# Kernel optimization log

Hardware: AMD Instinct MI355X
Metric: run time of the kernel (lower is better)

## Reference

```python
import jax, jax.numpy as jnp
import numpy as np

H = 1024        # bridge_hidden_dim
NH = 16         # num_attention_heads
HD = H // NH    # head_dim = 64
B, S = 4, 1024
PHYS_W = 0.2
CONS_W = 0.15


def setup_inputs() -> dict:
    key = jax.random.key(0)
    ks = jax.random.split(key, 16)
    sc = 0.02
    return {
        "cnn_features": jax.random.normal(ks[0], (B, S, H), jnp.float32),
        "llm_features": jax.random.normal(ks[1], (B, S, H), jnp.float32),
        "Wq": jax.random.normal(ks[2], (H, H), jnp.float32) * sc,
        "bq": jnp.zeros((H,), jnp.float32),
        "Wk": jax.random.normal(ks[3], (H, H), jnp.float32) * sc,
        "bk": jnp.zeros((H,), jnp.float32),
        "Wv": jax.random.normal(ks[4], (H, H), jnp.float32) * sc,
        "bv": jnp.zeros((H,), jnp.float32),
        "Wo": jax.random.normal(ks[5], (H, H), jnp.float32) * sc,
        "bo": jnp.zeros((H,), jnp.float32),
        "ln_g": jnp.ones((H,), jnp.float32),
        "ln_b": jnp.zeros((H,), jnp.float32),
        "e_energy": jax.random.normal(ks[6], (H,), jnp.float32),
        "e_mass": jax.random.normal(ks[7], (H,), jnp.float32),
        "e_momentum": jax.random.normal(ks[8], (H,), jnp.float32),
    }


def _layernorm(x, g, b, eps=1e-5):
    mu = jnp.mean(x, axis=-1, keepdims=True)
    var = jnp.var(x, axis=-1, keepdims=True)
    return (x - mu) * jax.lax.rsqrt(var + eps) * g + b


def _split_heads(x):
    b, s, _ = x.shape
    return x.reshape(b, s, NH, HD).transpose(0, 2, 1, 3)  # [b, h, s, d]


def _physics_attention(q_in, k_in, v_in, Wq, bq, Wk, bk, Wv, bv, Wo, bo, ln_g, ln_b):
    # q_in: [b, sq, H]; k_in == v_in: [b, sk, H] with sq == sk (required by bias math)
    Q = _split_heads(q_in @ Wq.T + bq)  # [b,h,s,d]
    K = _split_heads(k_in @ Wk.T + bk)
    V = _split_heads(v_in @ Wv.T + bv)
    scores = jnp.einsum('bhqd,bhkd->bhqk', Q, K) / jnp.sqrt(jnp.float32(HD))
    # physics constraints (broadcast [b,h,s,1] over key axis)
    energy_bias = jnp.sum(Q * K, axis=-1, keepdims=True) * PHYS_W
    mass_bias = jnp.mean(Q + K, axis=-1, keepdims=True) * CONS_W
    scores = scores + energy_bias + mass_bias
    attn = jax.nn.softmax(scores, axis=-1)  # dropout is identity in eval
    att = jnp.einsum('bhqk,bhkd->bhqd', attn, V)
    b, h, s, d = att.shape
    att = att.transpose(0, 2, 1, 3).reshape(b, s, h * d)
    out = att @ Wo.T + bo
    return _layernorm(q_in + out, ln_g, ln_b)


def reference(cnn_features, llm_features, Wq, bq, Wk, bk, Wv, bv, Wo, bo,
              ln_g, ln_b, e_energy, e_mass, e_momentum):
    b = cnn_features.shape[0]
    phys = jnp.stack([e_energy, e_mass, e_momentum], axis=0)  # [3, H]
    phys = jnp.broadcast_to(phys[None], (b, 3, H))
    aug_cnn = jnp.concatenate([cnn_features, phys], axis=1)  # [b, S+3, H]
    aug_llm = jnp.concatenate([llm_features, phys], axis=1)
    cnn_att = _physics_attention(aug_cnn, aug_llm, aug_llm,
                                 Wq, bq, Wk, bk, Wv, bv, Wo, bo, ln_g, ln_b)
    llm_att = _physics_attention(aug_llm, aug_cnn, aug_cnn,
                                 Wq, bq, Wk, bk, Wv, bv, Wo, bo, ln_g, ln_b)
    cnn_out = cnn_att[:, :cnn_features.shape[1], :]
    llm_out = llm_att[:, :llm_features.shape[1], :]
    return (cnn_out, llm_out)
```

## Files before the change

kernel.cpp:

```cpp
#include <hip/hip_runtime.h>
#include <stdint.h>

#define SA 1027
#define MROWS 8216
#define MPAD 8448
#define SPAD 1088
#define ATTM 8192

typedef __attribute__((ext_vector_type(8))) short short8;
typedef __attribute__((ext_vector_type(4))) float f32x4;
typedef __attribute__((ext_vector_type(2))) unsigned int u32x2;

typedef const __attribute__((address_space(1))) uint8_t* gas1;
typedef __attribute__((address_space(3))) uint8_t* las3;

__device__ __forceinline__ void gload16(const void* g, void* l){
  __builtin_amdgcn_global_load_lds((gas1)g, (las3)l, 16, 0, 0);
}

__device__ __forceinline__ uint16_t f2bf(float f){
  uint32_t x = __builtin_bit_cast(uint32_t, f);
  x = (x + 0x7fffu + ((x >> 16) & 1u)) >> 16;
  return (uint16_t)x;
}
__device__ __forceinline__ float bf2f(uint16_t u){
  uint32_t x = ((uint32_t)u) << 16;
  return __builtin_bit_cast(float, x);
}

__device__ __forceinline__ f32x4 mfma16(short8 a, short8 b, f32x4 c){
  return __builtin_amdgcn_mfma_f32_16x16x32_bf16(a, b, c, 0, 0, 0);
}

#define QSCALE 0.18033688011112042f

__global__ __launch_bounds__(256) void prep_wb(
    const float* __restrict__ Wq, const float* __restrict__ Wk,
    const float* __restrict__ Wv, const float* __restrict__ Wo,
    const float* __restrict__ bq, const float* __restrict__ bk,
    const float* __restrict__ bv, const float* __restrict__ bo,
    uint16_t* __restrict__ W, float* __restrict__ bias){
  const int gid = blockIdx.x*256 + threadIdx.x;
  if (gid < 1048576){
    const int w = gid >> 18;
    const int off = (gid & 262143) << 2;
    const float* src = (w==0) ? Wq : (w==1) ? Wk : (w==2) ? Wv : Wo;
    const float4 v = *(const float4*)(src + off);
    ushort4 u;
    u.x = f2bf(v.x); u.y = f2bf(v.y); u.z = f2bf(v.z); u.w = f2bf(v.w);
    *(ushort4*)(W + ((size_t)w << 20) + off) = u;
  } else if (gid < 1048576 + 1024){
    const int i = (gid - 1048576) << 2;
    const int w = i >> 10;
    const int off = i & 1023;
    const float* src = (w==0) ? bq : (w==1) ? bk : (w==2) ? bv : bo;
    *(float4*)(bias + i) = *(const float4*)(src + off);
  }
}

__global__ __launch_bounds__(256) void prep_X(
    const float* __restrict__ cnn, const float* __restrict__ llm,
    const float* __restrict__ ee, const float* __restrict__ em,
    const float* __restrict__ ep, uint16_t* __restrict__ X){
  const int row = blockIdx.x;
  const int c4 = threadIdx.x << 2;
  float4 v = {0.f,0.f,0.f,0.f};
  if (row < MROWS){
    const int cb = row / SA;
    const int s = row - cb*SA;
    const int c = cb >> 2, b = cb & 3;
    const float* src;
    if (s < 1024) src = (c ? llm : cnn) + ((size_t)(b*1024 + s))*1024 + c4;
    else src = ((s == 1024) ? ee : (s == 1025) ? em : ep) + c4;
    v = *(const float4*)src;
  }
  ushort4 u;
  u.x = f2bf(v.x); u.y = f2bf(v.y); u.z = f2bf(v.z); u.w = f2bf(v.w);
  *(ushort4*)(X + (size_t)row*1024 + c4) = u;
}

__global__ __launch_bounds__(512) void gemm256k(
    const uint16_t* __restrict__ A, const uint16_t* __restrict__ B,
    const float* __restrict__ bias, uint16_t* __restrict__ C,
    int K, int lda, int ldb, int ldc, int nbn, float qscale, int qcols){
  extern __shared__ uint8_t lds[];
  const int tid = threadIdx.x;
  const int lane = tid & 63, wid = tid >> 6;
  const int l15 = lane & 15, l4 = lane >> 4;
  const int wm = wid >> 2, wn = wid & 3;
  const int nwg = gridDim.x;
  const int q8 = nwg >> 3, r8 = nwg & 7;
  const int xcd = blockIdx.x & 7, loc = blockIdx.x >> 3;
  const int wg = (xcd < r8 ? xcd*(q8+1) : r8*(q8+1) + (xcd-r8)*q8) + loc;
  const int bm = wg / nbn, bn = wg % nbn;

  const uint16_t* Ag = A + (size_t)bm*256*lda;
  const uint16_t* Bg = B + (size_t)bn*256*ldb;

  const int srow8 = lane >> 3;
  const int gch = (lane & 7) ^ srow8;
  const int c0 = wid*2, c1 = c0 + 1;
  const size_t ga0 = (size_t)(c0*8 + srow8)*lda + gch*8;
  const size_t ga1 = (size_t)(c1*8 + srow8)*lda + gch*8;
  const size_t gb0 = (size_t)(c0*8 + srow8)*ldb + gch*8;
  const size_t gb1 = (size_t)(c1*8 + srow8)*ldb + gch*8;

#define STG_A(buf, H, kt) do { \
    gload16(Ag + (size_t)(H)*128*lda + (size_t)(kt)*64 + ga0, lds + (buf)*65536 + (H)*16384 + c0*1024); \
    gload16(Ag + (size_t)(H)*128*lda + (size_t)(kt)*64 + ga1, lds + (buf)*65536 + (H)*16384 + c1*1024); \
  } while(0)
#define STG_B(buf, H, kt) do { \
    gload16(Bg + (size_t)(H)*128*ldb + (size_t)(kt)*64 + gb0, lds + (buf)*65536 + 32768 + (H)*16384 + c0*1024); \
    gload16(Bg + (size_t)(H)*128*ldb + (size_t)(kt)*64 + gb1, lds + (buf)*65536 + 32768 + (H)*16384 + c1*1024); \
  } while(0)

  int koff[2];
  koff[0] = (l4*16) ^ ((l15 & 7) << 4);
  koff[1] = (64 + l4*16) ^ ((l15 & 7) << 4);
  const int arow = (wm*128 + l15) * 128;
  const int brow = (wn*64 + l15) * 128;

  f32x4 acc[8][4];
  #pragma unroll
  for (int i = 0; i < 8; ++i)
    #pragma unroll
    for (int j = 0; j < 4; ++j) acc[i][j] = (f32x4){0.f,0.f,0.f,0.f};

  const int NT = K >> 6;
  STG_A(0,0,0); STG_A(0,1,0); STG_B(0,0,0); STG_B(0,1,0);
  STG_B(1,0,1); STG_B(1,1,1);
  asm volatile("s_waitcnt vmcnt(4)" ::: "memory");
  __builtin_amdgcn_s_barrier();

  for (int s = 0; s < NT; ++s){
    const int b = s & 1;
    const uint8_t* La = lds + b*65536;
    const uint8_t* Lb = La + 32768;
    const int sn1 = (s+1 < NT) ? s+1 : s;
    const int sn2 = (s+2 < NT) ? s+2 : s;
    const int nb = b ^ 1;
    short8 af[4][2], bf0[2][2], bf1[2][2];

    #pragma unroll
    for (int i = 0; i < 4; ++i){
      af[i][0] = *(const short8*)(La + arow + i*2048 + koff[0]);
      af[i][1] = *(const short8*)(La + arow + i*2048 + koff[1]);
    }
    #pragma unroll
    for (int j = 0; j < 2; ++j){
      bf0[j][0] = *(const short8*)(Lb + brow + j*2048 + koff[0]);
      bf0[j][1] = *(const short8*)(Lb + brow + j*2048 + koff[1]);
    }
    STG_A(nb, 0, sn1);
    __builtin_amdgcn_s_barrier();
    asm volatile("s_waitcnt lgkmcnt(0)" ::: "memory");
    __builtin_amdgcn_sched_barrier(0);
    __builtin_amdgcn_s_setprio(1);
    #pragma unroll
    for (int i = 0; i < 4; ++i)
      #pragma unroll
      for (int j = 0; j < 2; ++j)
        acc[i][j] = mfma16(af[i][1], bf0[j][1], mfma16(af[i][0], bf0[j][0], acc[i][j]));
    __builtin_amdgcn_s_setprio(0);
    __builtin_amdgcn_s_barrier();

    #pragma unroll
    for (int j = 0; j < 2; ++j){
      bf1[j][0] = *(const short8*)(Lb + brow + (j+2)*2048 + koff[0]);
      bf1[j][1] = *(const short8*)(Lb + brow + (j+2)*2048 + koff[1]);
    }
    STG_A(nb, 1, sn1);
    __builtin_amdgcn_s_barrier();
    asm volatile("s_waitcnt lgkmcnt(0)" ::: "memory");
    __builtin_amdgcn_sched_barrier(0);
    __builtin_amdgcn_s_setprio(1);
    #pragma unroll
    for (int i = 0; i < 4; ++i)
      #pragma unroll
      for (int j = 0; j < 2; ++j)
        acc[i][j+2] = mfma16(af[i][1], bf1[j][1], mfma16(af[i][0], bf1[j][0], acc[i][j+2]));
    __builtin_amdgcn_s_setprio(0);
    __builtin_amdgcn_s_barrier();

    #pragma unroll
    for (int i = 0; i < 4; ++i){
      af[i][0] = *(const short8*)(La + 8192 + arow + i*2048 + koff[0]);
      af[i][1] = *(const short8*)(La + 8192 + arow + i*2048 + koff[1]);
    }
    STG_B(b, 0, sn2);
    __builtin_amdgcn_s_barrier();
    asm volatile("s_waitcnt lgkmcnt(0)" ::: "memory");
    __builtin_amdgcn_sched_barrier(0);
    __builtin_amdgcn_s_setprio(1);
    #pragma unroll
    for (int i = 0; i < 4; ++i)
      #pragma unroll
      for (int j = 0; j < 2; ++j)
        acc[i+4][j+2] = mfma16(af[i][1], bf1[j][1], mfma16(af[i][0], bf1[j][0], acc[i+4][j+2]));
    __builtin_amdgcn_s_setprio(0);
    __builtin_amdgcn_s_barrier();

    STG_B(b, 1, sn2);
    __builtin_amdgcn_s_barrier();
    __builtin_amdgcn_s_setprio(1);
    #pragma unroll
    for (int i = 0; i < 4; ++i)
      #pragma unroll
      for (int j = 0; j < 2; ++j)
        acc[i+4][j] = mfma16(af[i][1], bf0[j][1], mfma16(af[i][0], bf0[j][0], acc[i+4][j]));
    __builtin_amdgcn_s_setprio(0);
    asm volatile("s_waitcnt vmcnt(4)" ::: "memory");
    __builtin_amdgcn_s_barrier();
  }

  #pragma unroll
  for (int j = 0; j < 4; ++j){
    const int n = bn*256 + wn*64 + j*16 + l15;
    const float bb = bias[n];
    const float sc = (n < qcols) ? qscale : 1.0f;
    #pragma unroll
    for (int i = 0; i < 8; ++i){
      const size_t m0 = (size_t)bm*256 + wm*128 + i*16 + l4*4;
      #pragma unroll
      for (int r = 0; r < 4; ++r)
        C[(m0 + r)*ldc + n] = f2bf((acc[i][j][r] + bb) * sc);
    }
  }
#undef STG_A
#undef STG_B
}

__global__ __launch_bounds__(256) void vtrans(
    const uint16_t* __restrict__ Y, uint16_t* __restrict__ Vt){
  __shared__ uint16_t t[64][65];
  const int bid = blockIdx.x;
  const int st = bid % 17, cbh = bid / 17;
  const int s0 = st*64;
  const int tid = threadIdx.x;
  const int a = tid >> 2, g = tid & 3;
  const int cb = cbh >> 4, h = cbh & 15;
  const int s = s0 + a;
  short8 v0 = {0,0,0,0,0,0,0,0}, v1 = {0,0,0,0,0,0,0,0};
  if (s < SA){
    const uint16_t* p = Y + ((size_t)cb*SA + s)*3072 + 2048 + h*64 + g*16;
    v0 = *(const short8*)p;
    v1 = *(const short8*)(p + 8);
  }
  #pragma unroll
  for (int i=0;i<8;i++){ t[a][g*16+i] = (uint16_t)v0[i]; t[a][g*16+8+i] = (uint16_t)v1[i]; }
  __syncthreads();
  short8 w0, w1;
  #pragma unroll
  for (int i=0;i<8;i++){ w0[i] = (short)t[g*16+i][a]; w1[i] = (short)t[g*16+8+i][a]; }
  uint16_t* o = Vt + ((size_t)cbh*64 + a)*SPAD + s0 + g*16;
  *(short8*)o = w0;
  *(short8*)(o + 8) = w1;
}

__global__ __launch_bounds__(256, 4) void attn_k(
    const uint16_t* __restrict__ Y, const uint16_t* __restrict__ Vt,
    uint16_t* __restrict__ att){
  __shared__ __align__(16) uint8_t smK[16384];
  __shared__ __align__(16) uint8_t smV[16384];
  __shared__ __align__(16) uint8_t smP[8192];
  const int tid = threadIdx.x;
  const int lane = tid & 63, wid = tid >> 6;
  const int l15 = lane & 15, l4 = lane >> 4;
  const int i = blockIdx.x;
  const int inst = (i & 7) * 16 + (i >> 6);
  const int qb = (i >> 3) & 7;
  const int h = inst & 15, cb = inst >> 4;
  const size_t yrow0 = (size_t)cb * SA;
  const int q0 = qb * 128 + wid * 32;
  const size_t vbase = (size_t)inst * 64 * SPAD;
  const uint16_t* Yk = Y + yrow0 * 3072 + 1024 + h * 64;

  short8 qf[2][2];
  #pragma unroll
  for (int u = 0; u < 2; ++u){
    const uint16_t* p = Y + (yrow0 + q0 + u*16 + l15) * 3072 + h * 64 + l4 * 8;
    qf[u][0] = *(const short8*)p;
    qf[u][1] = *(const short8*)(p + 32);
  }

  f32x4 o0[4], o1[4];
  float psum0 = 0.f, psum1 = 0.f;
  #pragma unroll
  for (int d = 0; d < 4; ++d){ o0[d] = (f32x4){0,0,0,0}; o1[d] = (f32x4){0,0,0,0}; }

  int koff[2], pwo[4];
  #pragma unroll
  for (int kk = 0; kk < 2; ++kk)
    koff[kk] = (l15*128 + kk*64 + l4*16) ^ ((l15 & 7) << 4);
  #pragma unroll
  for (int nt = 0; nt < 4; ++nt)
    pwo[nt] = (l15*128 + nt*32 + l4*8) ^ ((l15 & 7) << 4);
  uint8_t* const pb = smP + wid * 2048;

  const int srow = lane >> 3, schunk = lane & 7;
  #pragma unroll
  for (int j = 0; j < 2; ++j){
    const int cj = wid*2 + j;
    const int row = cj*8 + srow;
    const int gch = schunk ^ (row & 7);
    gload16(Yk + (size_t)row * 3072 + gch*8, smK + cj*1024);
    gload16(Vt + vbase + (size_t)row * SPAD + gch*8, smV + cj*1024);
  }
  __syncthreads();

  int cur = 0;
  for (int kt = 0; kt < 17; ++kt){
    if (kt < 16){
      const int s1n = (kt + 1) * 64;
      const int nb = (cur ^ 1) * 8192;
      #pragma unroll
      for (int j = 0; j < 2; ++j){
        const int cj = wid*2 + j;
        const int row = cj*8 + srow;
        const int gch = schunk ^ (row & 7);
        gload16(Yk + (size_t)(s1n + row) * 3072 + gch*8, smK + nb + cj*1024);
        gload16(Vt + vbase + (size_t)row * SPAD + s1n + gch*8, smV + nb + cj*1024);
      }
    }
    const uint8_t* bK = smK + cur * 8192;
    const uint8_t* bV = smV + cur * 8192;

    f32x4 sa[4], sb[4];
    #pragma unroll
    for (int nt = 0; nt < 4; ++nt){
      const short8 k0 = *(const short8*)(bK + nt*2048 + koff[0]);
      const short8 k1 = *(const short8*)(bK + nt*2048 + koff[1]);
      sa[nt] = mfma16(k1, qf[0][1], mfma16(k0, qf[0][0], (f32x4){0,0,0,0}));
      sb[nt] = mfma16(k1, qf[1][1], mfma16(k0, qf[1][0], (f32x4){0,0,0,0}));
    }
    if (kt == 16){
      #pragma unroll
      for (int nt = 0; nt < 4; ++nt)
        #pragma unroll
        for (int r = 0; r < 4; ++r){
          if (nt*16 + l4*4 + r >= 3){ sa[nt][r] = -3e38f; sb[nt][r] = -3e38f; }
        }
    }
    #pragma unroll
    for (int nt = 0; nt < 4; ++nt){
      const float p0 = __builtin_amdgcn_exp2f(sa[nt][0]);
      const float p1 = __builtin_amdgcn_exp2f(sa[nt][1]);
      const float p2 = __builtin_amdgcn_exp2f(sa[nt][2]);
      const float p3 = __builtin_amdgcn_exp2f(sa[nt][3]);
      psum0 += (p0 + p1) + (p2 + p3);
      uint32_t w0, w1;
      asm("v_cvt_pk_bf16_f32 %0, %1, %2" : "=v"(w0) : "v"(p0), "v"(p1));
      asm("v_cvt_pk_bf16_f32 %0, %1, %2" : "=v"(w1) : "v"(p2), "v"(p3));
      *(u32x2*)(pb + pwo[nt]) = (u32x2){w0, w1};
    }
    short8 vf[4][2];
    #pragma unroll
    for (int dt = 0; dt < 4; ++dt){
      vf[dt][0] = *(const short8*)(bV + dt*2048 + koff[0]);
      vf[dt][1] = *(const short8*)(bV + dt*2048 + koff[1]);
    }
    #pragma unroll
    for (int kk = 0; kk < 2; ++kk){
      const short8 pf = *(const short8*)(pb + koff[kk]);
      #pragma unroll
      for (int dt = 0; dt < 4; ++dt)
        o0[dt] = mfma16(pf, vf[dt][kk], o0[dt]);
    }
    #pragma unroll
    for (int nt = 0; nt < 4; ++nt){
      const float p0 = __builtin_amdgcn_exp2f(sb[nt][0]);
      const float p1 = __builtin_amdgcn_exp2f(sb[nt][1]);
      const float p2 = __builtin_amdgcn_exp2f(sb[nt][2]);
      const float p3 = __builtin_amdgcn_exp2f(sb[nt][3]);
      psum1 += (p0 + p1) + (p2 + p3);
      uint32_t w0, w1;
      asm("v_cvt_pk_bf16_f32 %0, %1, %2" : "=v"(w0) : "v"(p0), "v"(p1));
      asm("v_cvt_pk_bf16_f32 %0, %1, %2" : "=v"(w1) : "v"(p2), "v"(p3));
      *(u32x2*)(pb + pwo[nt]) = (u32x2){w0, w1};
    }
    #pragma unroll
    for (int kk = 0; kk < 2; ++kk){
      const short8 pf = *(const short8*)(pb + koff[kk]);
      #pragma unroll
      for (int dt = 0; dt < 4; ++dt)
        o1[dt] = mfma16(pf, vf[dt][kk], o1[dt]);
    }
    __syncthreads();
    cur ^= 1;
  }

  psum0 += __shfl_xor(psum0, 16); psum0 += __shfl_xor(psum0, 32);
  psum1 += __shfl_xor(psum1, 16); psum1 += __shfl_xor(psum1, 32);
  const size_t arow0 = (size_t)cb * 1024 + q0;
  #pragma unroll
  for (int r = 0; r < 4; ++r){
    const float inv0 = 1.f / __shfl(psum0, l4*4 + r);
    const float inv1 = 1.f / __shfl(psum1, l4*4 + r);
    #pragma unroll
    for (int dt = 0; dt < 4; ++dt){
      att[(arow0 + l4*4 + r)*1024 + h*64 + dt*16 + l15] = f2bf(o0[dt][r] * inv0);
      att[(arow0 + 16 + l4*4 + r)*1024 + h*64 + dt*16 + l15] = f2bf(o1[dt][r] * inv1);
    }
  }
}

__global__ __launch_bounds__(256) void ln_out(
    const uint16_t* __restrict__ Op, const float* __restrict__ cnn,
    const float* __restrict__ llm, const float* __restrict__ g,
    const float* __restrict__ b, float* __restrict__ out){
  const int row = blockIdx.x;
  const int c = row >> 12, bq = row & 4095;
  const int tid = threadIdx.x;
  const ushort4 u = *(const ushort4*)(Op + (size_t)row*1024 + (tid<<2));
  const float4 rv = *(const float4*)((c ? llm : cnn) + (size_t)bq*1024 + (tid<<2));
  const float x0 = bf2f(u.x) + rv.x;
  const float x1 = bf2f(u.y) + rv.y;
  const float x2 = bf2f(u.z) + rv.z;
  const float x3 = bf2f(u.w) + rv.w;
  float s1 = x0+x1+x2+x3;
  float s2 = x0*x0+x1*x1+x2*x2+x3*x3;
  #pragma unroll
  for (int m=1;m<64;m<<=1){ s1 += __shfl_xor(s1,m); s2 += __shfl_xor(s2,m); }
  __shared__ float r1[4], r2[4];
  const int wid = tid >> 6, lane = tid & 63;
  if (lane == 0){ r1[wid] = s1; r2[wid] = s2; }
  __syncthreads();
  s1 = r1[0]+r1[1]+r1[2]+r1[3];
  s2 = r2[0]+r2[1]+r2[2]+r2[3];
  const float mu = s1 * 0.0009765625f;
  const float var = s2 * 0.0009765625f - mu*mu;
  const float rs = rsqrtf(var + 1e-5f);
  const float4 gv = *(const float4*)(g + (tid<<2));
  const float4 bv = *(const float4*)(b + (tid<<2));
  float4 ov;
  ov.x = (x0 - mu)*rs*gv.x + bv.x;
  ov.y = (x1 - mu)*rs*gv.y + bv.y;
  ov.z = (x2 - mu)*rs*gv.z + bv.z;
  ov.w = (x3 - mu)*rs*gv.w + bv.w;
  *(float4*)(out + ((size_t)c << 22) + (size_t)bq*1024 + (tid<<2)) = ov;
}

extern "C" void kernel_launch(void* const* d_in, const int* in_sizes, int n_in,
                              void* d_out, int out_size, void* d_ws, size_t ws_size,
                              hipStream_t stream){
  const float* cnn = (const float*)d_in[0];
  const float* llm = (const float*)d_in[1];
  const float* Wq  = (const float*)d_in[2];
  const float* bq  = (const float*)d_in[3];
  const float* Wk  = (const float*)d_in[4];
  const float* bk  = (const float*)d_in[5];
  const float* Wv  = (const float*)d_in[6];
  const float* bv  = (const float*)d_in[7];
  const float* Wo  = (const float*)d_in[8];
  const float* bo  = (const float*)d_in[9];
  const float* lng = (const float*)d_in[10];
  const float* lnb = (const float*)d_in[11];
  const float* ee  = (const float*)d_in[12];
  const float* em  = (const float*)d_in[13];
  const float* ep  = (const float*)d_in[14];

  uint8_t* ws = (uint8_t*)d_ws;
  uint16_t* X    = (uint16_t*)(ws + 0);
  uint16_t* W    = (uint16_t*)(ws + 17301504);
  float*    bias = (float*)   (ws + 25690112);
  uint16_t* Y    = (uint16_t*)(ws + 25706496);
  uint16_t* Vt   = (uint16_t*)(ws + 77611008);
  uint16_t* att  = X;
  uint16_t* Op   = Y;
  float* out = (float*)d_out;

  hipFuncSetAttribute((const void*)gemm256k,
                      hipFuncAttributeMaxDynamicSharedMemorySize, 131072);

  prep_wb<<<4100, 256, 0, stream>>>(Wq, Wk, Wv, Wo, bq, bk, bv, bo, W, bias);
  prep_X<<<MPAD, 256, 0, stream>>>(cnn, llm, ee, em, ep, X);
  gemm256k<<<396, 512, 131072, stream>>>(X, W, bias, Y, 1024, 1024, 1024, 3072, 12, QSCALE, 1024);
  vtrans<<<128*17, 256, 0, stream>>>(Y, Vt);
  attn_k<<<1024, 256, 0, stream>>>(Y, Vt, att);
  gemm256k<<<128, 512, 131072, stream>>>(att, W + 3145728, bias + 3072, Op, 1024, 1024, 1024, 1024, 4, 1.0f, 0);
  ln_out<<<ATTM, 256, 0, stream>>>(Op, cnn, llm, lng, lnb, out);
}
```

Before: 184.1 us.

## Fuse V transpose into QKV GEMM epilogue and split physics rows into separate kernel

The QKV GEMM moves from 256x256 to 256x128 tiles, which gives more workgroups. Its epilogue now writes Q/K into a 2048-wide buffer and V directly in transposed layout, so the separate vtrans kernel is removed. The three physics token rows are computed by a small dedicated GEMV kernel, which shrinks the main GEMM M dimension to exactly 8192 with no padding. The attention kernel uses 512-thread blocks covering 256 queries each to share K/V staging across more waves. This trades a larger per-block footprint and an extra tiny launch for one fewer full pass over V.

```diff
diff --git a/kernel.cpp b/kernel.cpp
--- a/kernel.cpp
+++ b/kernel.cpp
@@ -2,10 +2,7 @@
 #include <stdint.h>
 
 #define SA 1027
-#define MROWS 8216
-#define MPAD 8448
 #define SPAD 1088
-#define ATTM 8192
 
 typedef __attribute__((ext_vector_type(8))) short short8;
 typedef __attribute__((ext_vector_type(4))) float f32x4;
@@ -60,29 +57,53 @@
 
 __global__ __launch_bounds__(256) void prep_X(
     const float* __restrict__ cnn, const float* __restrict__ llm,
-    const float* __restrict__ ee, const float* __restrict__ em,
-    const float* __restrict__ ep, uint16_t* __restrict__ X){
+    uint16_t* __restrict__ X){
   const int row = blockIdx.x;
   const int c4 = threadIdx.x << 2;
-  float4 v = {0.f,0.f,0.f,0.f};
-  if (row < MROWS){
-    const int cb = row / SA;
-    const int s = row - cb*SA;
-    const int c = cb >> 2, b = cb & 3;
-    const float* src;
-    if (s < 1024) src = (c ? llm : cnn) + ((size_t)(b*1024 + s))*1024 + c4;
-    else src = ((s == 1024) ? ee : (s == 1025) ? em : ep) + c4;
-    v = *(const float4*)src;
-  }
+  const int cb = row >> 10, s = row & 1023;
+  const int c = cb >> 2, b = cb & 3;
+  const float4 v = *(const float4*)((c ? llm : cnn) + ((size_t)(b*1024 + s))*1024 + c4);
   ushort4 u;
   u.x = f2bf(v.x); u.y = f2bf(v.y); u.z = f2bf(v.z); u.w = f2bf(v.w);
   *(ushort4*)(X + (size_t)row*1024 + c4) = u;
 }
 
-__global__ __launch_bounds__(512) void gemm256k(
+__global__ __launch_bounds__(256) void phys_qkv(
+    const float* __restrict__ ee, const float* __restrict__ em,
+    const float* __restrict__ ep, const uint16_t* __restrict__ W,
+    const float* __restrict__ bias, uint16_t* __restrict__ Yqk,
+    uint16_t* __restrict__ Vt){
+  __shared__ float xs[1024];
+  const int t = blockIdx.x >> 3;
+  const int col = 1024 + (blockIdx.x & 7)*256 + threadIdx.x;
+  const float* e = (t==0) ? ee : (t==1) ? em : ep;
+  for (int k = threadIdx.x; k < 1024; k += 256) xs[k] = bf2f(f2bf(e[k]));
+  __syncthreads();
+  const uint16_t* wr = W + (size_t)col*1024;
+  float acc = 0.f;
+  for (int k = 0; k < 1024; k += 8){
+    const short8 w8 = *(const short8*)(wr + k);
+    #pragma unroll
+    for (int u = 0; u < 8; ++u) acc += bf2f((uint16_t)w8[u]) * xs[k+u];
+  }
+  const uint16_t o = f2bf(acc + bias[col]);
+  if (col < 2048){
+    #pragma unroll
+    for (int cb = 0; cb < 8; ++cb)
+      Yqk[((size_t)cb*SA + 1024 + t)*2048 + col] = o;
+  } else {
+    const int hd = col - 2048;
+    #pragma unroll
+    for (int cb = 0; cb < 8; ++cb)
+      Vt[((size_t)(cb*1024 + hd))*SPAD + 1024 + t] = o;
+  }
+}
+
+__global__ __launch_bounds__(512) void gemm256x128(
     const uint16_t* __restrict__ A, const uint16_t* __restrict__ B,
     const float* __restrict__ bias, uint16_t* __restrict__ C,
-    int K, int lda, int ldb, int ldc, int nbn, float qscale, int qcols){
+    uint16_t* __restrict__ Vt, int K, int lda, int ldb, int ldc,
+    int nbn, int mode, float qscale){
   extern __shared__ uint8_t lds[];
   const int tid = threadIdx.x;
   const int lane = tid & 63, wid = tid >> 6;
@@ -95,7 +116,7 @@
   const int bm = wg / nbn, bn = wg % nbn;
 
   const uint16_t* Ag = A + (size_t)bm*256*lda;
-  const uint16_t* Bg = B + (size_t)bn*256*ldb;
+  const uint16_t* Bg = B + (size_t)bn*128*ldb;
 
   const int srow8 = lane >> 3;
   const int gch = (lane & 7) ^ srow8;
@@ -106,50 +127,45 @@
   const size_t gb1 = (size_t)(c1*8 + srow8)*ldb + gch*8;
 
 #define STG_A(buf, H, kt) do { \
-    gload16(Ag + (size_t)(H)*128*lda + (size_t)(kt)*64 + ga0, lds + (buf)*65536 + (H)*16384 + c0*1024); \
-    gload16(Ag + (size_t)(H)*128*lda + (size_t)(kt)*64 + ga1, lds + (buf)*65536 + (H)*16384 + c1*1024); \
+    gload16(Ag + (size_t)(H)*128*lda + (size_t)(kt)*64 + ga0, lds + (buf)*49152 + (H)*16384 + c0*1024); \
+    gload16(Ag + (size_t)(H)*128*lda + (size_t)(kt)*64 + ga1, lds + (buf)*49152 + (H)*16384 + c1*1024); \
   } while(0)
-#define STG_B(buf, H, kt) do { \
-    gload16(Bg + (size_t)(H)*128*ldb + (size_t)(kt)*64 + gb0, lds + (buf)*65536 + 32768 + (H)*16384 + c0*1024); \
-    gload16(Bg + (size_t)(H)*128*ldb + (size_t)(kt)*64 + gb1, lds + (buf)*65536 + 32768 + (H)*16384 + c1*1024); \
+#define STG_B(buf, kt) do { \
+    gload16(Bg + (size_t)(kt)*64 + gb0, lds + (buf)*49152 + 32768 + c0*1024); \
+    gload16(Bg + (size_t)(kt)*64 + gb1, lds + (buf)*49152 + 32768 + c1*1024); \
   } while(0)
 
   int koff[2];
   koff[0] = (l4*16) ^ ((l15 & 7) << 4);
   koff[1] = (64 + l4*16) ^ ((l15 & 7) << 4);
-  const int arow = (wm*128 + l15) * 128;
-  const int brow = (wn*64 + l15) * 128;
-
-  f32x4 acc[8][4];
-  #pragma unroll
-  for (int i = 0; i < 8; ++i)
-    #pragma unroll
-    for (int j = 0; j < 4; ++j) acc[i][j] = (f32x4){0.f,0.f,0.f,0.f};
+  const int abase = wm*16384 + l15*128;
+  const int bbase = 32768 + (wn*32 + l15)*128;
+
+  f32x4 acc[8][2];
+  #pragma unroll
+  for (int i = 0; i < 8; ++i){ acc[i][0] = (f32x4){0,0,0,0}; acc[i][1] = (f32x4){0,0,0,0}; }
 
   const int NT = K >> 6;
-  STG_A(0,0,0); STG_A(0,1,0); STG_B(0,0,0); STG_B(0,1,0);
-  STG_B(1,0,1); STG_B(1,1,1);
-  asm volatile("s_waitcnt vmcnt(4)" ::: "memory");
+  STG_A(0,0,0); STG_A(0,1,0); STG_B(0,0); STG_B(1,1);
+  asm volatile("s_waitcnt vmcnt(2)" ::: "memory");
   __builtin_amdgcn_s_barrier();
 
   for (int s = 0; s < NT; ++s){
-    const int b = s & 1;
-    const uint8_t* La = lds + b*65536;
-    const uint8_t* Lb = La + 32768;
+    const int b = s & 1, nb = b ^ 1;
+    const uint8_t* L = lds + b*49152;
     const int sn1 = (s+1 < NT) ? s+1 : s;
     const int sn2 = (s+2 < NT) ? s+2 : s;
-    const int nb = b ^ 1;
-    short8 af[4][2], bf0[2][2], bf1[2][2];
+    short8 af[4][2], bfr[2][2];
 
     #pragma unroll
     for (int i = 0; i < 4; ++i){
-      af[i][0] = *(const short8*)(La + arow + i*2048 + koff[0]);
-      af[i][1] = *(const short8*)(La + arow + i*2048 + koff[1]);
+      af[i][0] = *(const short8*)(L + abase + i*2048 + koff[0]);
+      af[i][1] = *(const short8*)(L + abase + i*2048 + koff[1]);
     }
     #pragma unroll
     for (int j = 0; j < 2; ++j){
-      bf0[j][0] = *(const short8*)(Lb + brow + j*2048 + koff[0]);
-      bf0[j][1] = *(const short8*)(Lb + brow + j*2048 + koff[1]);
+      bfr[j][0] = *(const short8*)(L + bbase + j*2048 + koff[0]);
+      bfr[j][1] = *(const short8*)(L + bbase + j*2048 + koff[1]);
     }
     STG_A(nb, 0, sn1);
     __builtin_amdgcn_s_barrier();
@@ -160,16 +176,17 @@
     for (int i = 0; i < 4; ++i)
       #pragma unroll
       for (int j = 0; j < 2; ++j)
-        acc[i][j] = mfma16(af[i][1], bf0[j][1], mfma16(af[i][0], bf0[j][0], acc[i][j]));
+        acc[i][j] = mfma16(af[i][1], bfr[j][1], mfma16(af[i][0], bfr[j][0], acc[i][j]));
     __builtin_amdgcn_s_setprio(0);
     __builtin_amdgcn_s_barrier();
 
     #pragma unroll
-    for (int j = 0; j < 2; ++j){
-      bf1[j][0] = *(const short8*)(Lb + brow + (j+2)*2048 + koff[0]);
-      bf1[j][1] = *(const short8*)(Lb + brow + (j+2)*2048 + koff[1]);
+    for (int i = 0; i < 4; ++i){
+      af[i][0] = *(const short8*)(L + abase + 8192 + i*2048 + koff[0]);
+      af[i][1] = *(const short8*)(L + abase + 8192 + i*2048 + koff[1]);
     }
     STG_A(nb, 1, sn1);
+    STG_B(b, sn2);
     __builtin_amdgcn_s_barrier();
     asm volatile("s_waitcnt lgkmcnt(0)" ::: "memory");
     __builtin_amdgcn_sched_barrier(0);
@@ -178,107 +195,74 @@
     for (int i = 0; i < 4; ++i)
       #pragma unroll
       for (int j = 0; j < 2; ++j)
-        acc[i][j+2] = mfma16(af[i][1], bf1[j][1], mfma16(af[i][0], bf1[j][0], acc[i][j+2]));
+        acc[i+4][j] = mfma16(af[i][1], bfr[j][1], mfma16(af[i][0], bfr[j][0], acc[i+4][j]));
     __builtin_amdgcn_s_setprio(0);
+    asm volatile("s_waitcnt vmcnt(2)" ::: "memory");
     __builtin_amdgcn_s_barrier();
-
-    #pragma unroll
-    for (int i = 0; i < 4; ++i){
-      af[i][0] = *(const short8*)(La + 8192 + arow + i*2048 + koff[0]);
-      af[i][1] = *(const short8*)(La + 8192 + arow + i*2048 + koff[1]);
-    }
-    STG_B(b, 0, sn2);
-    __builtin_amdgcn_s_barrier();
-    asm volatile("s_waitcnt lgkmcnt(0)" ::: "memory");
-    __builtin_amdgcn_sched_barrier(0);
-    __builtin_amdgcn_s_setprio(1);
-    #pragma unroll
-    for (int i = 0; i < 4; ++i)
-      #pragma unroll
-      for (int j = 0; j < 2; ++j)
-        acc[i+4][j+2] = mfma16(af[i][1], bf1[j][1], mfma16(af[i][0], bf1[j][0], acc[i+4][j+2]));
-    __builtin_amdgcn_s_setprio(0);
-    __builtin_amdgcn_s_barrier();
-
-    STG_B(b, 1, sn2);
-    __builtin_amdgcn_s_barrier();
-    __builtin_amdgcn_s_setprio(1);
-    #pragma unroll
-    for (int i = 0; i < 4; ++i)
-      #pragma unroll
-      for (int j = 0; j < 2; ++j)
-        acc[i+4][j] = mfma16(af[i][1], bf0[j][1], mfma16(af[i][0], bf0[j][0], acc[i+4][j]));
-    __builtin_amdgcn_s_setprio(0);
-    asm volatile("s_waitcnt vmcnt(4)" ::: "memory");
-    __builtin_amdgcn_s_barrier();
-  }
-
-  #pragma unroll
-  for (int j = 0; j < 4; ++j){
-    const int n = bn*256 + wn*64 + j*16 + l15;
+  }
+
+  #pragma unroll
+  for (int j = 0; j < 2; ++j){
+    const int n = bn*128 + wn*32 + j*16 + l15;
     const float bb = bias[n];
-    const float sc = (n < qcols) ? qscale : 1.0f;
-    #pragma unroll
-    for (int i = 0; i < 8; ++i){
-      const size_t m0 = (size_t)bm*256 + wm*128 + i*16 + l4*4;
-      #pragma unroll
-      for (int r = 0; r < 4; ++r)
-        C[(m0 + r)*ldc + n] = f2bf((acc[i][j][r] + bb) * sc);
+    if (mode == 0){
+      #pragma unroll
+      for (int i = 0; i < 8; ++i){
+        const size_t m0 = (size_t)bm*256 + wm*128 + i*16 + l4*4;
+        #pragma unroll
+        for (int r = 0; r < 4; ++r)
+          C[(m0 + r)*ldc + n] = f2bf(acc[i][j][r] + bb);
+      }
+    } else if (bn < 16){
+      const float sc = (n < 1024) ? qscale : 1.0f;
+      #pragma unroll
+      for (int i = 0; i < 8; ++i){
+        const int m0 = bm*256 + wm*128 + i*16 + l4*4;
+        #pragma unroll
+        for (int r = 0; r < 4; ++r){
+          const int m = m0 + r;
+          const size_t row = (size_t)(m >> 10)*SA + (m & 1023);
+          C[row*2048 + n] = f2bf((acc[i][j][r] + bb) * sc);
+        }
+      }
+    } else {
+      const int hd = n - 2048;
+      #pragma unroll
+      for (int i = 0; i < 8; ++i){
+        const int m0 = bm*256 + wm*128 + i*16 + l4*4;
+        const size_t vrow = (size_t)(m0 >> 10)*1024 + hd;
+        const uint32_t w0 = (uint32_t)f2bf(acc[i][j][0] + bb) | ((uint32_t)f2bf(acc[i][j][1] + bb) << 16);
+        const uint32_t w1 = (uint32_t)f2bf(acc[i][j][2] + bb) | ((uint32_t)f2bf(acc[i][j][3] + bb) << 16);
+        *(u32x2*)(Vt + vrow*SPAD + (m0 & 1023)) = (u32x2){w0, w1};
+      }
     }
   }
 #undef STG_A
 #undef STG_B
 }
 
-__global__ __launch_bounds__(256) void vtrans(
-    const uint16_t* __restrict__ Y, uint16_t* __restrict__ Vt){
-  __shared__ uint16_t t[64][65];
-  const int bid = blockIdx.x;
-  const int st = bid % 17, cbh = bid / 17;
-  const int s0 = st*64;
-  const int tid = threadIdx.x;
-  const int a = tid >> 2, g = tid & 3;
-  const int cb = cbh >> 4, h = cbh & 15;
-  const int s = s0 + a;
-  short8 v0 = {0,0,0,0,0,0,0,0}, v1 = {0,0,0,0,0,0,0,0};
-  if (s < SA){
-    const uint16_t* p = Y + ((size_t)cb*SA + s)*3072 + 2048 + h*64 + g*16;
-    v0 = *(const short8*)p;
-    v1 = *(const short8*)(p + 8);
-  }
-  #pragma unroll
-  for (int i=0;i<8;i++){ t[a][g*16+i] = (uint16_t)v0[i]; t[a][g*16+8+i] = (uint16_t)v1[i]; }
-  __syncthreads();
-  short8 w0, w1;
-  #pragma unroll
-  for (int i=0;i<8;i++){ w0[i] = (short)t[g*16+i][a]; w1[i] = (short)t[g*16+8+i][a]; }
-  uint16_t* o = Vt + ((size_t)cbh*64 + a)*SPAD + s0 + g*16;
-  *(short8*)o = w0;
-  *(short8*)(o + 8) = w1;
-}
-
-__global__ __launch_bounds__(256, 4) void attn_k(
-    const uint16_t* __restrict__ Y, const uint16_t* __restrict__ Vt,
+__global__ __launch_bounds__(512, 4) void attn_k(
+    const uint16_t* __restrict__ Yqk, const uint16_t* __restrict__ Vt,
     uint16_t* __restrict__ att){
   __shared__ __align__(16) uint8_t smK[16384];
   __shared__ __align__(16) uint8_t smV[16384];
-  __shared__ __align__(16) uint8_t smP[8192];
+  __shared__ __align__(16) uint8_t smP[16384];
   const int tid = threadIdx.x;
   const int lane = tid & 63, wid = tid >> 6;
   const int l15 = lane & 15, l4 = lane >> 4;
   const int i = blockIdx.x;
-  const int inst = (i & 7) * 16 + (i >> 6);
-  const int qb = (i >> 3) & 7;
+  const int inst = (i & 7)*16 + ((i >> 3) & 15);
+  const int qb = i >> 7;
   const int h = inst & 15, cb = inst >> 4;
   const size_t yrow0 = (size_t)cb * SA;
-  const int q0 = qb * 128 + wid * 32;
+  const int q0 = qb*256 + wid*32;
   const size_t vbase = (size_t)inst * 64 * SPAD;
-  const uint16_t* Yk = Y + yrow0 * 3072 + 1024 + h * 64;
+  const uint16_t* Yk = Yqk + yrow0*2048 + 1024 + h*64;
 
   short8 qf[2][2];
   #pragma unroll
   for (int u = 0; u < 2; ++u){
-    const uint16_t* p = Y + (yrow0 + q0 + u*16 + l15) * 3072 + h * 64 + l4 * 8;
+    const uint16_t* p = Yqk + (yrow0 + q0 + u*16 + l15)*2048 + h*64 + l4*8;
     qf[u][0] = *(const short8*)p;
     qf[u][1] = *(const short8*)(p + 32);
   }
@@ -295,35 +279,27 @@
   #pragma unroll
   for (int nt = 0; nt < 4; ++nt)
     pwo[nt] = (l15*128 + nt*32 + l4*8) ^ ((l15 & 7) << 4);
-  uint8_t* const pb = smP + wid * 2048;
+  uint8_t* const pb = smP + wid*2048;
 
   const int srow = lane >> 3, schunk = lane & 7;
-  #pragma unroll
-  for (int j = 0; j < 2; ++j){
-    const int cj = wid*2 + j;
-    const int row = cj*8 + srow;
-    const int gch = schunk ^ (row & 7);
-    gload16(Yk + (size_t)row * 3072 + gch*8, smK + cj*1024);
-    gload16(Vt + vbase + (size_t)row * SPAD + gch*8, smV + cj*1024);
+  const int strow = wid*8 + srow;
+  const int sgch = schunk ^ srow;
+  {
+    gload16(Yk + (size_t)strow*2048 + sgch*8, smK + wid*1024);
+    gload16(Vt + vbase + (size_t)strow*SPAD + sgch*8, smV + wid*1024);
   }
   __syncthreads();
 
   int cur = 0;
   for (int kt = 0; kt < 17; ++kt){
     if (kt < 16){
-      const int s1n = (kt + 1) * 64;
-      const int nb = (cur ^ 1) * 8192;
-      #pragma unroll
-      for (int j = 0; j < 2; ++j){
-        const int cj = wid*2 + j;
-        const int row = cj*8 + srow;
-        const int gch = schunk ^ (row & 7);
-        gload16(Yk + (size_t)(s1n + row) * 3072 + gch*8, smK + nb + cj*1024);
-        gload16(Vt + vbase + (size_t)row * SPAD + s1n + gch*8, smV + nb + cj*1024);
-      }
-    }
-    const uint8_t* bK = smK + cur * 8192;
-    const uint8_t* bV = smV + cur * 8192;
+      const int s1n = (kt + 1)*64;
+      const int nb = (cur ^ 1)*8192;
+      gload16(Yk + (size_t)(s1n + strow)*2048 + sgch*8, smK + nb + wid*1024);
+      gload16(Vt + vbase + (size_t)strow*SPAD + s1n + sgch*8, smV + nb + wid*1024);
+    }
+    const uint8_t* bK = smK + cur*8192;
+    const uint8_t* bV = smV + cur*8192;
 
     f32x4 sa[4], sb[4];
     #pragma unroll
@@ -391,7 +367,7 @@
 
   psum0 += __shfl_xor(psum0, 16); psum0 += __shfl_xor(psum0, 32);
   psum1 += __shfl_xor(psum1, 16); psum1 += __shfl_xor(psum1, 32);
-  const size_t arow0 = (size_t)cb * 1024 + q0;
+  const size_t arow0 = (size_t)cb*1024 + q0;
   #pragma unroll
   for (int r = 0; r < 4; ++r){
     const float inv0 = 1.f / __shfl(psum0, l4*4 + r);
@@ -461,22 +437,24 @@
 
   uint8_t* ws = (uint8_t*)d_ws;
   uint16_t* X    = (uint16_t*)(ws + 0);
-  uint16_t* W    = (uint16_t*)(ws + 17301504);
-  float*    bias = (float*)   (ws + 25690112);
-  uint16_t* Y    = (uint16_t*)(ws + 25706496);
-  uint16_t* Vt   = (uint16_t*)(ws + 77611008);
+  uint16_t* W    = (uint16_t*)(ws + 16777216);
+  float*    bias = (float*)   (ws + 25165824);
+  uint16_t* Yqk  = (uint16_t*)(ws + 25182208);
+  uint16_t* Vt   = (uint16_t*)(ws + 59785216);
   uint16_t* att  = X;
-  uint16_t* Op   = Y;
+  uint16_t* Op   = Yqk;
   float* out = (float*)d_out;
 
-  hipFuncSetAttribute((const void*)gemm256k,
-                      hipFuncAttributeMaxDynamicSharedMemorySize, 131072);
+  hipFuncSetAttribute((const void*)gemm256x128,
+                      hipFuncAttributeMaxDynamicSharedMemorySize, 98304);
 
   prep_wb<<<4100, 256, 0, stream>>>(Wq, Wk, Wv, Wo, bq, bk, bv, bo, W, bias);
-  prep_X<<<MPAD, 256, 0, stream>>>(cnn, llm, ee, em, ep, X);
-  gemm256k<<<396, 512, 131072, stream>>>(X, W, bias, Y, 1024, 1024, 1024, 3072, 12, QSCALE, 1024);
-  vtrans<<<128*17, 256, 0, stream>>>(Y, Vt);
-  attn_k<<<1024, 256, 0, stream>>>(Y, Vt, att);
-  gemm256k<<<128, 512, 131072, stream>>>(att, W + 3145728, bias + 3072, Op, 1024, 1024, 1024, 1024, 4, 1.0f, 0);
-  ln_out<<<ATTM, 256, 0, stream>>>(Op, cnn, llm, lng, lnb, out);
-}
+  prep_X<<<8192, 256, 0, stream>>>(cnn, llm, X);
+  phys_qkv<<<24, 256, 0, stream>>>(ee, em, ep, W, bias, Yqk, Vt);
+  gemm256x128<<<768, 512, 98304, stream>>>(X, W, bias, Yqk, Vt,
+                                           1024, 1024, 1024, 2048, 24, 1, QSCALE);
+  attn_k<<<512, 512, 0, stream>>>(Yqk, Vt, att);
+  gemm256x128<<<256, 512, 98304, stream>>>(att, W + 3145728, bias + 3072, Op, Vt,
+                                           1024, 1024, 1024, 1024, 8, 0, 1.0f);
+  ln_out<<<8192, 256, 0, stream>>>(Op, cnn, llm, lng, lnb, out);
+}
```

Result: no change. 184.2 us (+0.0%).
